# Optimization experiments

Hardware: AMD Instinct MI355X
Metric: run time of the kernel (lower is better)

Reference implementation:

```python
import jax, jax.numpy as jnp
import numpy as np
from jax import lax

DIM = 512
HEADS = 8
DIM_HEAD = 64          # dim // 8
LANDMARKS = 256        # dim // 2
PINV_ITERS = 6
KERNEL = 33            # residual depthwise conv kernel (lucidrains default)
LN_EPS = 1e-5


def setup_inputs() -> dict:
    key = jax.random.key(0)
    ks = jax.random.split(key, 5)
    b, n = 4, 8192
    x = jax.random.normal(ks[0], (b, n, DIM), jnp.float32)
    ln_w = jnp.ones((DIM,), jnp.float32)
    ln_b = jnp.zeros((DIM,), jnp.float32)
    w_qkv = jax.random.normal(ks[1], (DIM, 3 * HEADS * DIM_HEAD), jnp.float32) * (DIM ** -0.5)
    w_out = jax.random.normal(ks[2], (HEADS * DIM_HEAD, DIM), jnp.float32) * (DIM ** -0.5)
    b_out = jnp.zeros((DIM,), jnp.float32)
    conv_w = jax.random.normal(ks[3], (HEADS, 1, KERNEL, 1), jnp.float32) * 0.05
    return {"x": x, "ln_w": ln_w, "ln_b": ln_b, "w_qkv": w_qkv,
            "w_out": w_out, "b_out": b_out, "conv_w": conv_w}


def _moore_penrose_pinv(a, iters):
    # iterative Moore-Penrose pseudoinverse (Ben-Israel/Cohen cubic scheme)
    abs_a = jnp.abs(a)
    # global max over all batch/head slices, matching torch.max(col)*torch.max(row)
    scale = jnp.max(abs_a.sum(-1)) * jnp.max(abs_a.sum(-2))
    z = jnp.swapaxes(a, -1, -2) / scale
    I = jnp.eye(a.shape[-1], dtype=a.dtype)
    for _ in range(iters):
        az = a @ z
        z = 0.25 * (z @ (13.0 * I - az @ (11.0 * I - az @ (7.0 * I - az))))
    return z


def reference(x, ln_w, ln_b, w_qkv, w_out, b_out, conv_w):
    b, n, d = x.shape
    h, dh, m = HEADS, DIM_HEAD, LANDMARKS
    # --- LayerNorm ---
    mu = jnp.mean(x, -1, keepdims=True)
    var = jnp.mean((x - mu) ** 2, -1, keepdims=True)
    xn = (x - mu) * lax.rsqrt(var + LN_EPS) * ln_w + ln_b
    # --- pad front so seq divisible by num_landmarks (static; 0 here) ---
    pad = (-n) % m
    xp = jnp.pad(xn, ((0, 0), (pad, 0), (0, 0)))
    npad = n + pad
    # --- qkv projections ---
    qkv = xp @ w_qkv                      # (b, npad, 3*h*dh)
    q, k, v = jnp.split(qkv, 3, axis=-1)
    to_heads = lambda t: t.reshape(b, npad, h, dh).transpose(0, 2, 1, 3)  # bhnd
    q = to_heads(q) * (dh ** -0.5)
    k = to_heads(k)
    v = to_heads(v)
    # --- landmarks: mean over contiguous blocks of length l ---
    l = npad // m
    q_l = q.reshape(b, h, m, l, dh).mean(3)   # (b,h,m,dh)
    k_l = k.reshape(b, h, m, l, dh).mean(3)
    # --- three similarity/softmax blocks ---
    a1 = jax.nn.softmax(jnp.einsum('bhid,bhjd->bhij', q, k_l), -1)   # (b,h,n,m)
    a2 = jax.nn.softmax(jnp.einsum('bhid,bhjd->bhij', q_l, k_l), -1) # (b,h,m,m)
    a3 = jax.nn.softmax(jnp.einsum('bhid,bhjd->bhij', q_l, k), -1)   # (b,h,m,n)
    out = (a1 @ _moore_penrose_pinv(a2, PINV_ITERS)) @ (a3 @ v)      # (b,h,n,dh)
    # --- depthwise conv residual on v along sequence axis ---
    res = lax.conv_general_dilated(
        v, conv_w, window_strides=(1, 1),
        padding=((KERNEL // 2, KERNEL // 2), (0, 0)),
        dimension_numbers=('NCHW', 'OIHW', 'NCHW'),
        feature_group_count=h)
    out = out + res
    # --- merge heads, output projection, strip pad (dropout = identity in eval) ---
    out = out.transpose(0, 2, 1, 3).reshape(b, npad, h * dh)
    out = out @ w_out + b_out
    out = out[:, npad - n:]
    # --- TransLayer residual ---
    return x + out
```

## Files before the change

### kernel.cpp

```cpp
#include <hip/hip_runtime.h>

#define DEV __device__ __forceinline__

typedef unsigned short u16;
typedef unsigned int   u32;
typedef u16   u16x8 __attribute__((ext_vector_type(8)));
typedef __bf16 bf16x8 __attribute__((ext_vector_type(8)));
typedef float f32x4 __attribute__((ext_vector_type(4)));

DEV float b2f(u16 u){ return __uint_as_float(((u32)u) << 16); }
DEV u16 f2b(float f){ u32 u = __float_as_uint(f); u32 r = (u + 0x7fffu + ((u >> 16) & 1u)) >> 16; return (u16)r; }

DEV f32x4 mfma16(u16x8 a, u16x8 b, f32x4 c){
  return __builtin_amdgcn_mfma_f32_16x16x32_bf16(
      __builtin_bit_cast(bf16x8, a), __builtin_bit_cast(bf16x8, b), c, 0, 0, 0);
}

DEV void gload16(const void* g, void* l){
  __builtin_amdgcn_global_load_lds(
      (const __attribute__((address_space(1))) u32*)g,
      (__attribute__((address_space(3))) u32*)l,
      16, 0, 0);
}

__global__ __launch_bounds__(256) void ln_kernel(const float* __restrict__ x,
                                                 const float* __restrict__ w,
                                                 const float* __restrict__ bb,
                                                 u16* __restrict__ xn,
                                                 float2* __restrict__ stats){
  int row = blockIdx.x;
  const float* xr = x + (size_t)row * 512;
  int t = threadIdx.x;
  float2 v = *(const float2*)(xr + t * 2);
  float s = v.x + v.y;
  float sq = v.x * v.x + v.y * v.y;
  #pragma unroll
  for(int off = 32; off; off >>= 1){ s += __shfl_xor(s, off, 64); sq += __shfl_xor(sq, off, 64); }
  __shared__ float rs[4], rq[4];
  int wv = t >> 6, ln = t & 63;
  if(ln == 0){ rs[wv] = s; rq[wv] = sq; }
  __syncthreads();
  s = rs[0] + rs[1] + rs[2] + rs[3];
  sq = rq[0] + rq[1] + rq[2] + rq[3];
  float mu = s * (1.f / 512.f);
  float var = sq * (1.f / 512.f) - mu * mu;
  float rstd = rsqrtf(var + 1e-5f);
  if(t == 0) stats[row] = make_float2(mu, rstd);
  float w0 = w[t * 2], w1 = w[t * 2 + 1], b0 = bb[t * 2], b1 = bb[t * 2 + 1];
  u16 u0 = f2b((v.x - mu) * rstd * w0 + b0);
  u16 u1 = f2b((v.y - mu) * rstd * w1 + b1);
  ((u32*)(xn + (size_t)row * 512))[t] = (u32)u0 | ((u32)u1 << 16);
}

__global__ __launch_bounds__(256) void xl_kernel(const float* __restrict__ x,
                                                 const float2* __restrict__ stats,
                                                 const float* __restrict__ w,
                                                 const float* __restrict__ bb,
                                                 float* __restrict__ xl){
  int blk = blockIdx.x;
  int b = blk >> 8, j = blk & 255;
  int t = threadIdx.x;
  int d0 = t * 2;
  float acc0 = 0.f, acc1 = 0.f;
  size_t row0 = (size_t)b * 8192 + (size_t)j * 32;
  for(int tt = 0; tt < 32; tt++){
    size_t row = row0 + tt;
    float2 st = stats[row];
    const float* xr = x + row * 512;
    float2 v = *(const float2*)(xr + d0);
    acc0 += (v.x - st.x) * st.y;
    acc1 += (v.y - st.x) * st.y;
  }
  float* dst = xl + (size_t)blk * 512;
  dst[d0]     = acc0 * (1.f / 32.f) * w[d0]     + bb[d0];
  dst[d0 + 1] = acc1 * (1.f / 32.f) * w[d0 + 1] + bb[d0 + 1];
}

__global__ __launch_bounds__(256) void prep_weights(const float* __restrict__ w_qkv,
                                                    const float* __restrict__ w_out,
                                                    u16* __restrict__ wqkvT,
                                                    u16* __restrict__ woutT,
                                                    float* __restrict__ wqkT){
  int idx = blockIdx.x * 256 + threadIdx.x;
  if(idx < 786432){
    int k = idx / 1536, n = idx - k * 1536;
    wqkvT[(size_t)n * 512 + k] = f2b(w_qkv[idx]);
  } else if(idx < 786432 + 262144){
    int i2 = idx - 786432;
    int k = i2 >> 9, n = i2 & 511;
    woutT[(size_t)n * 512 + k] = f2b(w_out[i2]);
  } else {
    int i3 = idx - 786432 - 262144;
    int n = i3 >> 9, k = i3 & 511;
    wqkT[i3] = w_qkv[(size_t)k * 1536 + n];
  }
}

__global__ __launch_bounds__(256) void vtrans_kernel(const u16* __restrict__ v,
                                                     u16* __restrict__ vt){
  __shared__ u16 tile[64][72];
  int bh = blockIdx.y, n0 = blockIdx.x * 64;
  int t = threadIdx.x;
  for(int s = t; s < 512; s += 256){
    int row = s >> 3, col = (s & 7) * 8;
    *(u16x8*)&tile[row][col] = *(const u16x8*)(v + ((size_t)bh * 8192 + n0 + row) * 64 + col);
  }
  __syncthreads();
  for(int s = t; s < 512; s += 256){
    int d = s >> 3, nc = (s & 7) * 8;
    u16x8 u;
    #pragma unroll
    for(int e = 0; e < 8; e++) u[e] = tile[nc + e][d];
    *(u16x8*)(vt + ((size_t)bh * 64 + d) * 8192 + n0 + nc) = u;
  }
}

template<int EPI>
__global__ __launch_bounds__(256) void gemm128(const u16* __restrict__ A,
                                               const u16* __restrict__ BT,
                                               u16* __restrict__ qo, u16* __restrict__ ko, u16* __restrict__ vo,
                                               const float* __restrict__ bout,
                                               const float* __restrict__ xres,
                                               float* __restrict__ dout){
  __shared__ u16 As[128 * 32];
  __shared__ u16 Bs[128 * 32];
  const int K = 512;
  int nby = gridDim.y;
  int nwg = gridDim.x * nby;
  int orig = blockIdx.y * gridDim.x + blockIdx.x;
  int cpx = nwg >> 3;
  int wg = (orig & 7) * cpx + (orig >> 3);
  int fx = wg / nby, fy = wg - fx * nby;
  int tb_m = fx * 128, tb_n = fy * 128;
  int tid = threadIdx.x, lane = tid & 63, w = tid >> 6;
  int wm = (w >> 1) * 64, wn = (w & 1) * 64;
  f32x4 acc[4][4] = {};
  int srow = tid >> 2, sk = (tid & 3) * 8;
  const u16* Ag = A + (size_t)(tb_m + srow) * K + sk;
  const u16* Bg = BT + (size_t)(tb_n + srow) * K + sk;
  u16* Al = As + tid * 8;
  u16* Bl = Bs + tid * 8;
  for(int kk = 0; kk < K; kk += 32){
    __syncthreads();
    gload16(Ag + kk, Al);
    gload16(Ag + kk + (size_t)64 * K, Al + 2048);
    gload16(Bg + kk, Bl);
    gload16(Bg + kk + (size_t)64 * K, Bl + 2048);
    __syncthreads();
    int r = lane & 15, ko2 = (lane >> 4) * 8;
    u16x8 af[4], bf[4];
    #pragma unroll
    for(int mi = 0; mi < 4; mi++) af[mi] = *(const u16x8*)&As[(wm + mi * 16 + r) * 32 + ko2];
    #pragma unroll
    for(int ni = 0; ni < 4; ni++) bf[ni] = *(const u16x8*)&Bs[(wn + ni * 16 + r) * 32 + ko2];
    #pragma unroll
    for(int mi = 0; mi < 4; mi++)
      #pragma unroll
      for(int ni = 0; ni < 4; ni++)
        acc[mi][ni] = mfma16(af[mi], bf[ni], acc[mi][ni]);
  }
  int r = lane & 15, rr = (lane >> 4) * 4;
  #pragma unroll
  for(int mi = 0; mi < 4; mi++)
    #pragma unroll
    for(int ni = 0; ni < 4; ni++){
      int col = tb_n + wn + ni * 16 + r;
      #pragma unroll
      for(int e = 0; e < 4; e++){
        int row = tb_m + wm + mi * 16 + rr + e;
        float val = acc[mi][ni][e];
        if(EPI == 0){
          int t3 = col >> 9, h = (col >> 6) & 7, dh = col & 63;
          int b = row >> 13, n = row & 8191;
          if(t3 == 0) val *= 0.125f;
          u16* dst = (t3 == 0 ? qo : (t3 == 1 ? ko : vo));
          dst[(((size_t)(b * 8 + h) * 8192) + n) * 64 + dh] = f2b(val);
        } else {
          val += bout[col] + xres[(size_t)row * 512 + col];
          dout[(size_t)row * 512 + col] = val;
        }
      }
    }
}

__global__ __launch_bounds__(256) void gemm_qlkl(const float* __restrict__ A,
                                                 const float* __restrict__ BT,
                                                 float* __restrict__ qlf,
                                                 float* __restrict__ klf,
                                                 u16* __restrict__ qlh, u16* __restrict__ qll,
                                                 u16* __restrict__ klh, u16* __restrict__ kll){
  __shared__ float As[64][17];
  __shared__ float Bs[64][17];
  int tb_m = blockIdx.x * 64, tb_n = blockIdx.y * 64;
  int tid = threadIdx.x;
  int ty = tid >> 4, tx = tid & 15;
  float acc[4][4] = {};
  int srow = tid >> 2, sseg = (tid & 3) * 4;
  const float* Ag = A + (size_t)(tb_m + srow) * 512 + sseg;
  const float* Bg = BT + (size_t)(tb_n + srow) * 512 + sseg;
  for(int kk = 0; kk < 512; kk += 16){
    __syncthreads();
    f32x4 a4 = *(const f32x4*)(Ag + kk);
    f32x4 b4 = *(const f32x4*)(Bg + kk);
    #pragma unroll
    for(int e = 0; e < 4; e++){ As[srow][sseg + e] = a4[e]; Bs[srow][sseg + e] = b4[e]; }
    __syncthreads();
    #pragma unroll
    for(int k2 = 0; k2 < 16; k2++){
      float a[4], b[4];
      #pragma unroll
      for(int i = 0; i < 4; i++) a[i] = As[ty * 4 + i][k2];
      #pragma unroll
      for(int jv = 0; jv < 4; jv++) b[jv] = Bs[tx * 4 + jv][k2];
      #pragma unroll
      for(int i = 0; i < 4; i++)
        #pragma unroll
        for(int jv = 0; jv < 4; jv++) acc[i][jv] += a[i] * b[jv];
    }
  }
  #pragma unroll
  for(int i = 0; i < 4; i++)
    #pragma unroll
    for(int jv = 0; jv < 4; jv++){
      int r = tb_m + ty * 4 + i;
      int c = tb_n + tx * 4 + jv;
      int b = r >> 8, jl = r & 255;
      float val = acc[i][jv];
      if(c < 512){
        float q = val * 0.125f;
        size_t qi = (((size_t)(b * 8 + (c >> 6)) * 256) + jl) * 64 + (c & 63);
        qlf[qi] = q;
        u16 hi = f2b(q);
        qlh[qi] = hi; qll[qi] = f2b(q - b2f(hi));
      } else {
        int c2 = c - 512;
        size_t ki = (((size_t)(b * 8 + (c2 >> 6)) * 256) + jl) * 64 + (c2 & 63);
        klf[ki] = val;
        u16 hi = f2b(val);
        klh[ki] = hi; kll[ki] = f2b(val - b2f(hi));
      }
    }
}

__global__ __launch_bounds__(256) void gemm_pinv_f32(const float* __restrict__ A,
                                                     const float* __restrict__ B,
                                                     float* __restrict__ C,
                                                     float dB, float sB, float osc){
  __shared__ float As[64][68];
  __shared__ float Bs[64][68];
  int bh = blockIdx.y;
  size_t base = (size_t)bh * 65536;
  int tb_m = (blockIdx.x >> 2) * 64, tb_n = (blockIdx.x & 3) * 64;
  int tid = threadIdx.x;
  int ty = tid >> 4, tx = tid & 15;
  float acc[4][4] = {};
  int arow = tid >> 2, acol = (tid & 3) * 16;
  int brow = tid >> 3, bcol = (tid & 7) * 8;
  const float* Ag = A + base + (size_t)(tb_m + arow) * 256 + acol;
  const float* Bg = B + base + (size_t)brow * 256 + tb_n + bcol;
  for(int kk = 0; kk < 256; kk += 64){
    f32x4 a[4];
    #pragma unroll
    for(int q = 0; q < 4; q++) a[q] = *(const f32x4*)(Ag + kk + q * 4);
    f32x4 b[2][2];
    #pragma unroll
    for(int rr = 0; rr < 2; rr++){
      const float* bp = Bg + (size_t)(kk + rr * 32) * 256;
      b[rr][0] = *(const f32x4*)bp;
      b[rr][1] = *(const f32x4*)(bp + 4);
    }
    __syncthreads();
    #pragma unroll
    for(int q = 0; q < 4; q++)
      #pragma unroll
      for(int e = 0; e < 4; e++)
        As[acol + q * 4 + e][arow] = a[q][e];
    #pragma unroll
    for(int rr = 0; rr < 2; rr++){
      int krow = kk + rr * 32 + brow;
      f32x4 v0, v1;
      #pragma unroll
      for(int e = 0; e < 4; e++){
        float t0 = sB * b[rr][0][e]; if(krow == tb_n + bcol + e)     t0 += dB;
        float t1 = sB * b[rr][1][e]; if(krow == tb_n + bcol + 4 + e) t1 += dB;
        v0[e] = t0; v1[e] = t1;
      }
      *(f32x4*)&Bs[rr * 32 + brow][bcol]     = v0;
      *(f32x4*)&Bs[rr * 32 + brow][bcol + 4] = v1;
    }
    __syncthreads();
    #pragma unroll
    for(int k2 = 0; k2 < 64; k2++){
      f32x4 av4 = *(const f32x4*)&As[k2][ty * 4];
      f32x4 bv4 = *(const f32x4*)&Bs[k2][tx * 4];
      #pragma unroll
      for(int i = 0; i < 4; i++)
        #pragma unroll
        for(int jv = 0; jv < 4; jv++) acc[i][jv] += av4[i] * bv4[jv];
    }
  }
  #pragma unroll
  for(int i = 0; i < 4; i++){
    int r = tb_m + ty * 4 + i;
    f32x4 ov;
    #pragma unroll
    for(int jv = 0; jv < 4; jv++) ov[jv] = osc * acc[i][jv];
    *(f32x4*)(C + base + (size_t)r * 256 + tb_n + tx * 4) = ov;
  }
}

__global__ __launch_bounds__(256) void a2_kernel(const float* __restrict__ qlf,
                                                 const float* __restrict__ klf,
                                                 float* __restrict__ a2){
  int i = blockIdx.x, bh = blockIdx.y, j = threadIdx.x;
  const float* qp = qlf + ((size_t)bh * 256 + i) * 64;
  const float* kp = klf + ((size_t)bh * 256 + j) * 64;
  float s = 0.f;
  #pragma unroll
  for(int d0 = 0; d0 < 16; d0++){
    f32x4 uq = *(const f32x4*)(qp + d0 * 4);
    f32x4 uk = *(const f32x4*)(kp + d0 * 4);
    #pragma unroll
    for(int e = 0; e < 4; e++) s += uq[e] * uk[e];
  }
  __shared__ float red[256];
  red[j] = s; __syncthreads();
  for(int off = 128; off; off >>= 1){ if(j < off) red[j] = fmaxf(red[j], red[j + off]); __syncthreads(); }
  float m = red[0]; __syncthreads();
  float p = expf(s - m);
  red[j] = p; __syncthreads();
  for(int off = 128; off; off >>= 1){ if(j < off) red[j] += red[j + off]; __syncthreads(); }
  float denom = red[0];
  a2[((size_t)bh * 256 + i) * 256 + j] = p / denom;
}

__global__ __launch_bounds__(256) void scale_kernel(const float* __restrict__ a2, u32* __restrict__ maxes){
  int bh = blockIdx.x, t = threadIdx.x;
  const float* p = a2 + (size_t)bh * 65536;
  float cs = 0.f, rs = 0.f;
  for(int i = 0; i < 256; i++) cs += p[i * 256 + t];
  for(int j = 0; j < 256; j++) rs += p[t * 256 + j];
  __shared__ float rc[256], rr[256];
  rc[t] = cs; rr[t] = rs; __syncthreads();
  for(int off = 128; off; off >>= 1){
    if(t < off){ rc[t] = fmaxf(rc[t], rc[t + off]); rr[t] = fmaxf(rr[t], rr[t + off]); }
    __syncthreads();
  }
  if(t == 0){
    atomicMax(&maxes[0], __float_as_uint(rc[0]));
    atomicMax(&maxes[1], __float_as_uint(rr[0]));
  }
}

__global__ __launch_bounds__(256) void z0_kernel(const float* __restrict__ a2,
                                                 float* __restrict__ z,
                                                 const u32* __restrict__ maxes){
  __shared__ float tile[64][65];
  float inv = 1.f / (__uint_as_float(maxes[0]) * __uint_as_float(maxes[1]));
  int bh = blockIdx.z;
  int i0 = blockIdx.x * 64, j0 = blockIdx.y * 64;
  const float* src = a2 + (size_t)bh * 65536;
  float* dst = z + (size_t)bh * 65536;
  for(int s = threadIdx.x; s < 1024; s += 256){
    int r = s >> 4, c4 = (s & 15) * 4;
    f32x4 v = *(const f32x4*)(src + (size_t)(i0 + r) * 256 + j0 + c4);
    #pragma unroll
    for(int e = 0; e < 4; e++) tile[r][c4 + e] = v[e];
  }
  __syncthreads();
  for(int s = threadIdx.x; s < 1024; s += 256){
    int jr = s >> 4, c4 = (s & 15) * 4;
    f32x4 v;
    #pragma unroll
    for(int e = 0; e < 4; e++) v[e] = tile[c4 + e][jr] * inv;
    *(f32x4*)(dst + (size_t)(j0 + jr) * 256 + i0 + c4) = v;
  }
}

template<int MODE>
__global__ __launch_bounds__(256) void flash_kernel(
    const u16* __restrict__ Aex,
    const u16* __restrict__ Ah_, const u16* __restrict__ Al_,
    const u16* __restrict__ Bh_, const u16* __restrict__ Bl_,
    const u16* __restrict__ Vh_, const u16* __restrict__ Vl_,
    u16* __restrict__ o,
    float* __restrict__ pacc, float* __restrict__ plo){
  extern __shared__ char smem[];
  u32 (*pbuf)[32][35] = (u32(*)[32][35])smem;
  u16 (*ksh)[72] = (u16(*)[72])(smem + 17920);
  u16 (*vsh)[72] = (u16(*)[72])(smem + 17920 + 9216);
  u16 (*ksl)[72] = (u16(*)[72])(smem + 17920 + 2 * 9216);
  u16 (*vsl)[72] = (u16(*)[72])(smem + 17920 + 3 * 9216);

  int tid = threadIdx.x;
  int w = tid >> 6, lane = tid & 63;
  int lr = lane & 15, lg = lane >> 4;
  int bh = blockIdx.y;
  int rowbase = blockIdx.x * 128 + w * 32;
  constexpr int NT = (MODE == 0) ? 4 : 8;
  int kbase = (MODE == 0) ? 0 : blockIdx.z * 512;
  int srow = tid >> 2, sseg = (tid & 3) * 16;

  u16x8 afh[2][2], afl[2][2];
  #pragma unroll
  for(int mi = 0; mi < 2; mi++)
    #pragma unroll
    for(int ks = 0; ks < 2; ks++){
      int r = rowbase + mi * 16 + lr;
      if(MODE == 0){
        afh[mi][ks] = *(const u16x8*)(Aex + ((size_t)bh * 8192 + r) * 64 + ks * 32 + lg * 8);
      } else {
        size_t idx = ((size_t)bh * 256 + r) * 64 + ks * 32 + lg * 8;
        afh[mi][ks] = *(const u16x8*)(Ah_ + idx);
        afl[mi][ks] = *(const u16x8*)(Al_ + idx);
      }
    }

  f32x4 pv[2][4] = {};
  float l[2][4] = {};

  for(int t = 0; t < NT; t++){
    int koff = t * 64;
    __syncthreads();
    if(MODE == 0){
      size_t kix = ((size_t)bh * 256 + koff + srow) * 64 + sseg;
      *(u16x8*)&ksh[srow][sseg]     = *(const u16x8*)(Bh_ + kix);
      *(u16x8*)&ksh[srow][sseg + 8] = *(const u16x8*)(Bh_ + kix + 8);
      *(u16x8*)&ksl[srow][sseg]     = *(const u16x8*)(Bl_ + kix);
      *(u16x8*)&ksl[srow][sseg + 8] = *(const u16x8*)(Bl_ + kix + 8);
      size_t vix = ((size_t)bh * 64 + srow) * 256 + koff + sseg;
      *(u16x8*)&vsh[srow][sseg]     = *(const u16x8*)(Vh_ + vix);
      *(u16x8*)&vsh[srow][sseg + 8] = *(const u16x8*)(Vh_ + vix + 8);
      *(u16x8*)&vsl[srow][sseg]     = *(const u16x8*)(Vl_ + vix);
      *(u16x8*)&vsl[srow][sseg + 8] = *(const u16x8*)(Vl_ + vix + 8);
    } else {
      size_t kix = ((size_t)bh * 8192 + kbase + koff + srow) * 64 + sseg;
      *(u16x8*)&ksh[srow][sseg]     = *(const u16x8*)(Bh_ + kix);
      *(u16x8*)&ksh[srow][sseg + 8] = *(const u16x8*)(Bh_ + kix + 8);
      size_t vix = ((size_t)bh * 64 + srow) * 8192 + kbase + koff + sseg;
      *(u16x8*)&vsh[srow][sseg]     = *(const u16x8*)(Vh_ + vix);
      *(u16x8*)&vsh[srow][sseg + 8] = *(const u16x8*)(Vh_ + vix + 8);
    }
    __syncthreads();
    #pragma unroll
    for(int half = 0; half < 2; half++){
      u16x8 bfh[2][2], bfl[2][2];
      #pragma unroll
      for(int ni = 0; ni < 2; ni++){
        int krow = half * 32 + ni * 16 + lr;
        #pragma unroll
        for(int ks = 0; ks < 2; ks++){
          bfh[ni][ks] = *(const u16x8*)&ksh[krow][ks * 32 + lg * 8];
          if(MODE == 0) bfl[ni][ks] = *(const u16x8*)&ksl[krow][ks * 32 + lg * 8];
        }
      }
      f32x4 sv[2][2];
      #pragma unroll
      for(int mi = 0; mi < 2; mi++)
        #pragma unroll
        for(int ni = 0; ni < 2; ni++) sv[mi][ni] = (f32x4){0.f, 0.f, 0.f, 0.f};
      #pragma unroll
      for(int ks = 0; ks < 2; ks++)
        #pragma unroll
        for(int mi = 0; mi < 2; mi++)
          #pragma unroll
          for(int ni = 0; ni < 2; ni++){
            sv[mi][ni] = mfma16(afh[mi][ks], bfh[ni][ks], sv[mi][ni]);
            if(MODE == 0) sv[mi][ni] = mfma16(afh[mi][ks], bfl[ni][ks], sv[mi][ni]);
            else          sv[mi][ni] = mfma16(afl[mi][ks], bfh[ni][ks], sv[mi][ni]);
          }
      #pragma unroll
      for(int mi = 0; mi < 2; mi++)
        #pragma unroll
        for(int ni = 0; ni < 2; ni++)
          #pragma unroll
          for(int e = 0; e < 4; e++){
            float p = __expf(sv[mi][ni][e]);
            l[mi][e] += p;
            u32 pb = __float_as_uint(p);
            u32 rb = pb + 0x7fffu + ((pb >> 16) & 1u);
            float hif = __uint_as_float(rb & 0xffff0000u);
            u32 lob = __float_as_uint(p - hif);
            pbuf[w][mi * 16 + lg * 4 + e][ni * 16 + lr] = __builtin_amdgcn_perm(lob, rb, 0x07060302u);
          }
      u16x8 pah[2], pal[2];
      #pragma unroll
      for(int mi = 0; mi < 2; mi++){
        u32 tv[8];
        #pragma unroll
        for(int e2 = 0; e2 < 8; e2++) tv[e2] = pbuf[w][mi * 16 + lr][lg * 8 + e2];
        u32* ph = (u32*)&pah[mi];
        u32* pl = (u32*)&pal[mi];
        #pragma unroll
        for(int q = 0; q < 4; q++){
          ph[q] = __builtin_amdgcn_perm(tv[2 * q + 1], tv[2 * q], 0x05040100u);
          pl[q] = __builtin_amdgcn_perm(tv[2 * q + 1], tv[2 * q], 0x07060302u);
        }
      }
      #pragma unroll
      for(int ni2 = 0; ni2 < 4; ni2++){
        int d = ni2 * 16 + lr;
        u16x8 vh = *(const u16x8*)&vsh[d][half * 32 + lg * 8];
        u16x8 vl;
        if(MODE == 0) vl = *(const u16x8*)&vsl[d][half * 32 + lg * 8];
        #pragma unroll
        for(int mi = 0; mi < 2; mi++){
          pv[mi][ni2] = mfma16(pah[mi], vh, pv[mi][ni2]);
          if(MODE == 0){
            pv[mi][ni2] = mfma16(pah[mi], vl, pv[mi][ni2]);
            pv[mi][ni2] = mfma16(pal[mi], vh, pv[mi][ni2]);
          } else {
            pv[mi][ni2] = mfma16(pal[mi], vh, pv[mi][ni2]);
          }
        }
      }
    }
  }
  #pragma unroll
  for(int mi = 0; mi < 2; mi++)
    #pragma unroll
    for(int e = 0; e < 4; e++){
      float lv = l[mi][e];
      #pragma unroll
      for(int off = 1; off < 16; off <<= 1) lv += __shfl_xor(lv, off, 64);
      l[mi][e] = lv;
    }
  #pragma unroll
  for(int mi = 0; mi < 2; mi++){
    #pragma unroll
    for(int e = 0; e < 4; e++){
      int row = rowbase + mi * 16 + lg * 4 + e;
      if(MODE == 0){
        float invl = 1.f / l[mi][e];
        int b = bh >> 3, h = bh & 7;
        #pragma unroll
        for(int ni2 = 0; ni2 < 4; ni2++){
          int col = ni2 * 16 + lr;
          size_t oi = ((size_t)b * 8192 + row) * 512 + h * 64 + col;
          o[oi] = f2b(pv[mi][ni2][e] * invl + b2f(o[oi]));
        }
      } else {
        #pragma unroll
        for(int ni2 = 0; ni2 < 4; ni2++){
          int col = ni2 * 16 + lr;
          pacc[(((size_t)blockIdx.z * 8192) + (size_t)bh * 256 + row) * 64 + col] = pv[mi][ni2][e];
        }
      }
    }
  }
  if(MODE == 1 && lr == 0){
    #pragma unroll
    for(int mi = 0; mi < 2; mi++)
      #pragma unroll
      for(int e = 0; e < 4; e++){
        int row = rowbase + mi * 16 + lg * 4 + e;
        plo[(size_t)blockIdx.z * 8192 + (size_t)bh * 256 + row] = l[mi][e];
      }
  }
}

__global__ __launch_bounds__(64) void a3v_merge(const float* __restrict__ pacc,
                                                const float* __restrict__ plo,
                                                float* __restrict__ av){
  int row = blockIdx.x, d = threadIdx.x;
  float L = 0.f, acc = 0.f;
  #pragma unroll
  for(int p = 0; p < 16; p++){
    L += plo[(size_t)p * 8192 + row];
    acc += pacc[((size_t)p * 8192 + row) * 64 + d];
  }
  av[(size_t)row * 64 + d] = acc / L;
}

__global__ __launch_bounds__(64) void zw_kernel(const float* __restrict__ z,
                                                const float* __restrict__ av,
                                                u16* __restrict__ wth, u16* __restrict__ wtl){
  int i = blockIdx.x & 255, bh = blockIdx.x >> 8, d = threadIdx.x;
  const float* zr = z + ((size_t)bh * 256 + i) * 256;
  const float* ab = av + (size_t)bh * 256 * 64;
  float s = 0.f;
  for(int j = 0; j < 256; j++) s += zr[j] * ab[j * 64 + d];
  size_t oi = ((size_t)bh * 64 + d) * 256 + i;
  u16 hi = f2b(s);
  wth[oi] = hi;
  wtl[oi] = f2b(s - b2f(hi));
}

__global__ __launch_bounds__(256) void conv_kernel(const u16* __restrict__ v,
                                                   const float* __restrict__ cw,
                                                   u16* __restrict__ o){
  __shared__ float wl[33];
  __shared__ float vt[64][104];
  int bh = blockIdx.y, b = bh >> 3, h = bh & 7;
  int r0 = blockIdx.x * 64;
  if(threadIdx.x < 33) wl[threadIdx.x] = cw[h * 33 + threadIdx.x];
  const u16* vb = v + (size_t)bh * 8192 * 64;
  for(int idx = threadIdx.x; idx < 768; idx += 256){
    int row = idx >> 3, c8 = (idx & 7) * 8;
    int gr = r0 - 16 + row;
    u16x8 u = {};
    if(gr >= 0 && gr < 8192) u = *(const u16x8*)(vb + (size_t)gr * 64 + c8);
    #pragma unroll
    for(int e = 0; e < 8; e++) vt[c8 + e][row] = b2f(u[e]);
  }
  __syncthreads();
  int d = threadIdx.x & 63, g = threadIdx.x >> 6;
  float vin[48];
  #pragma unroll
  for(int i = 0; i < 12; i++){
    f32x4 q4 = *(const f32x4*)&vt[d][g * 16 + i * 4];
    #pragma unroll
    for(int e = 0; e < 4; e++) vin[i * 4 + e] = q4[e];
  }
  float acc[16] = {};
  #pragma unroll
  for(int t = 0; t < 33; t++){
    float wt = wl[t];
    #pragma unroll
    for(int r = 0; r < 16; r++) acc[r] += wt * vin[r + t];
  }
  #pragma unroll
  for(int r = 0; r < 16; r++){
    size_t oi = ((size_t)b * 8192 + (r0 + g * 16 + r)) * 512 + h * 64 + d;
    o[oi] = f2b(acc[r]);
  }
}

extern "C" void kernel_launch(void* const* d_in, const int* in_sizes, int n_in,
                              void* d_out, int out_size, void* d_ws, size_t ws_size,
                              hipStream_t stream){
  (void)in_sizes; (void)n_in; (void)out_size; (void)ws_size;
  const float* x     = (const float*)d_in[0];
  const float* ln_w  = (const float*)d_in[1];
  const float* ln_b  = (const float*)d_in[2];
  const float* w_qkv = (const float*)d_in[3];
  const float* w_out = (const float*)d_in[4];
  const float* b_out = (const float*)d_in[5];
  const float* cw    = (const float*)d_in[6];
  float* out = (float*)d_out;

  char* base = (char*)d_ws;
  size_t off = 0;
  auto alloc = [&](size_t bytes)->void*{
    void* r = base + off; off += (bytes + 255) & ~(size_t)255; return r;
  };
  u16* xn      = (u16*)alloc(32768ull * 512 * 2);
  float2* stat = (float2*)alloc(32768ull * 8);
  u16* qb      = (u16*)alloc(32ull * 8192 * 64 * 2);
  u16* kb      = (u16*)alloc(32ull * 8192 * 64 * 2);
  u16* vb      = (u16*)alloc(32ull * 8192 * 64 * 2);
  u16* vtb     = (u16*)alloc(32ull * 8192 * 64 * 2);
  u16* wqkvT   = (u16*)alloc(1536ull * 512 * 2);
  u16* woutT   = (u16*)alloc(512ull * 512 * 2);
  float* wqkT  = (float*)alloc(1024ull * 512 * 4);
  float* xl    = (float*)alloc(1024ull * 512 * 4);
  float* qlf   = (float*)alloc(32ull * 256 * 64 * 4);
  float* klf   = (float*)alloc(32ull * 256 * 64 * 4);
  u16* qlh     = (u16*)alloc(32ull * 256 * 64 * 2);
  u16* qll     = (u16*)alloc(32ull * 256 * 64 * 2);
  u16* klh     = (u16*)alloc(32ull * 256 * 64 * 2);
  u16* kll     = (u16*)alloc(32ull * 256 * 64 * 2);
  float* a2b   = (float*)alloc(32ull * 65536 * 4);
  float* zA    = (float*)alloc(32ull * 65536 * 4);
  float* zB    = (float*)alloc(32ull * 65536 * 4);
  float* az    = (float*)alloc(32ull * 65536 * 4);
  float* x2    = (float*)alloc(32ull * 65536 * 4);
  float* x3    = (float*)alloc(32ull * 65536 * 4);
  float* av    = (float*)alloc(32ull * 256 * 64 * 4);
  u16* wth     = (u16*)alloc(32ull * 64 * 256 * 2);
  u16* wtl     = (u16*)alloc(32ull * 64 * 256 * 2);
  u32* scal    = (u32*)alloc(256);
  u16* ob = xn;
  float* pacc = zB;
  float* plo  = a2b;

  hipMemsetAsync(scal, 0, 8, stream);
  ln_kernel<<<32768, 256, 0, stream>>>(x, ln_w, ln_b, xn, stat);
  prep_weights<<<6144, 256, 0, stream>>>(w_qkv, w_out, wqkvT, woutT, wqkT);
  gemm128<0><<<dim3(256, 12), 256, 0, stream>>>(xn, wqkvT, qb, kb, vb, nullptr, nullptr, nullptr);
  vtrans_kernel<<<dim3(128, 32), 256, 0, stream>>>(vb, vtb);
  xl_kernel<<<1024, 256, 0, stream>>>(x, stat, ln_w, ln_b, xl);
  gemm_qlkl<<<dim3(16, 16), 256, 0, stream>>>(xl, wqkT, qlf, klf, qlh, qll, klh, kll);
  a2_kernel<<<dim3(256, 32), 256, 0, stream>>>(qlf, klf, a2b);
  scale_kernel<<<32, 256, 0, stream>>>(a2b, scal);
  z0_kernel<<<dim3(4, 4, 32), 256, 0, stream>>>(a2b, zA, scal);

  float* zP = zA; float* zQ = zB;
  for(int it = 0; it < 6; it++){
    gemm_pinv_f32<<<dim3(16, 32), 256, 0, stream>>>(a2b, zP, az, 0.f, 1.f, 1.f);
    gemm_pinv_f32<<<dim3(16, 32), 256, 0, stream>>>(az, az, x2, 7.f, -1.f, 1.f);
    gemm_pinv_f32<<<dim3(16, 32), 256, 0, stream>>>(az, x2, x3, 11.f, -1.f, 1.f);
    gemm_pinv_f32<<<dim3(16, 32), 256, 0, stream>>>(zP, x3, zQ, 13.f, -1.f, 0.25f);
    float* t1 = zP; zP = zQ; zQ = t1;
  }

  flash_kernel<1><<<dim3(2, 32, 16), 256, 36352, stream>>>(nullptr, qlh, qll, kb, nullptr, vtb, nullptr,
                                                           nullptr, pacc, plo);
  a3v_merge<<<8192, 64, 0, stream>>>(pacc, plo, av);
  zw_kernel<<<8192, 64, 0, stream>>>(zP, av, wth, wtl);
  conv_kernel<<<dim3(128, 32), 256, 0, stream>>>(vb, cw, ob);
  flash_kernel<0><<<dim3(64, 32), 256, 54784, stream>>>(qb, nullptr, nullptr, klh, kll, wth, wtl,
                                                        ob, nullptr, nullptr);
  gemm128<1><<<dim3(256, 4), 256, 0, stream>>>(ob, woutT, nullptr, nullptr, nullptr, b_out, x, out);
}
```

Measured before the change: 951.1 us.

## Run pinv GEMMs on bf16 MFMA with three-way split precision

```diff
diff --git a/kernel.cpp b/kernel.cpp
--- a/kernel.cpp
+++ b/kernel.cpp
@@ -4,12 +4,26 @@
 
 typedef unsigned short u16;
 typedef unsigned int   u32;
+typedef u16   u16x4 __attribute__((ext_vector_type(4)));
 typedef u16   u16x8 __attribute__((ext_vector_type(8)));
 typedef __bf16 bf16x8 __attribute__((ext_vector_type(8)));
 typedef float f32x4 __attribute__((ext_vector_type(4)));
 
 DEV float b2f(u16 u){ return __uint_as_float(((u32)u) << 16); }
 DEV u16 f2b(float f){ u32 u = __float_as_uint(f); u32 r = (u + 0x7fffu + ((u >> 16) & 1u)) >> 16; return (u16)r; }
+
+DEV void split3(float x, u16& h, u16& l, u16& l2){
+  u32 ub = __float_as_uint(x);
+  u32 rb = ub + 0x7fffu + ((ub >> 16) & 1u);
+  float hf = __uint_as_float(rb & 0xffff0000u);
+  float r1 = x - hf;
+  u32 u1 = __float_as_uint(r1);
+  u32 rb1 = u1 + 0x7fffu + ((u1 >> 16) & 1u);
+  float lf = __uint_as_float(rb1 & 0xffff0000u);
+  h = (u16)(rb >> 16);
+  l = (u16)(rb1 >> 16);
+  l2 = f2b(r1 - lf);
+}
 
 DEV f32x4 mfma16(u16x8 a, u16x8 b, f32x4 c){
   return __builtin_amdgcn_mfma_f32_16x16x32_bf16(
@@ -242,76 +256,87 @@
     }
 }
 
-__global__ __launch_bounds__(256) void gemm_pinv_f32(const float* __restrict__ A,
-                                                     const float* __restrict__ B,
-                                                     float* __restrict__ C,
-                                                     float dB, float sB, float osc){
-  __shared__ float As[64][68];
-  __shared__ float Bs[64][68];
+__global__ __launch_bounds__(256) void gemm_pinv_mfma(
+    const u16* __restrict__ Ah, const u16* __restrict__ Al, const u16* __restrict__ Al2,
+    const u16* __restrict__ Bh, const u16* __restrict__ Bl, const u16* __restrict__ Bl2,
+    u16* __restrict__ Ch, u16* __restrict__ Cl, u16* __restrict__ Cl2,
+    float dB, int bneg, float osc){
+  __shared__ u16 As_[3][64][40];
+  __shared__ u16 Bs_[3][64][40];
   int bh = blockIdx.y;
   size_t base = (size_t)bh * 65536;
   int tb_m = (blockIdx.x >> 2) * 64, tb_n = (blockIdx.x & 3) * 64;
-  int tid = threadIdx.x;
-  int ty = tid >> 4, tx = tid & 15;
-  float acc[4][4] = {};
-  int arow = tid >> 2, acol = (tid & 3) * 16;
-  int brow = tid >> 3, bcol = (tid & 7) * 8;
-  const float* Ag = A + base + (size_t)(tb_m + arow) * 256 + acol;
-  const float* Bg = B + base + (size_t)brow * 256 + tb_n + bcol;
-  for(int kk = 0; kk < 256; kk += 64){
-    f32x4 a[4];
-    #pragma unroll
-    for(int q = 0; q < 4; q++) a[q] = *(const f32x4*)(Ag + kk + q * 4);
-    f32x4 b[2][2];
-    #pragma unroll
-    for(int rr = 0; rr < 2; rr++){
-      const float* bp = Bg + (size_t)(kk + rr * 32) * 256;
-      b[rr][0] = *(const f32x4*)bp;
-      b[rr][1] = *(const f32x4*)(bp + 4);
-    }
-    __syncthreads();
-    #pragma unroll
-    for(int q = 0; q < 4; q++)
-      #pragma unroll
-      for(int e = 0; e < 4; e++)
-        As[acol + q * 4 + e][arow] = a[q][e];
-    #pragma unroll
-    for(int rr = 0; rr < 2; rr++){
-      int krow = kk + rr * 32 + brow;
-      f32x4 v0, v1;
+  int tid = threadIdx.x, lane = tid & 63, w = tid >> 6;
+  int lr = lane & 15, lg = lane >> 4;
+  int wm = (w >> 1) * 32, wn = (w & 1) * 32;
+  f32x4 acc[2][2] = {};
+  int arow = tid >> 2, akq = (tid & 3) * 8;
+  int bcol = tid & 63, bkq = tid >> 6;
+  u16 sx = bneg ? (u16)0x8000u : (u16)0;
+  size_t aoff = base + (size_t)(tb_m + arow) * 256 + akq;
+  size_t boff = base + (size_t)(tb_n + bcol);
+  for(int kk = 0; kk < 256; kk += 32){
+    u16x8 ra0 = *(const u16x8*)(Ah + aoff + kk);
+    u16x8 ra1 = *(const u16x8*)(Al + aoff + kk);
+    u16x8 ra2 = *(const u16x8*)(Al2 + aoff + kk);
+    u16x8 rb0, rb1, rb2;
+    #pragma unroll
+    for(int j = 0; j < 8; j++){
+      size_t bi = boff + (size_t)(kk + bkq * 8 + j) * 256;
+      rb0[j] = Bh[bi] ^ sx;
+      rb1[j] = Bl[bi] ^ sx;
+      rb2[j] = Bl2[bi] ^ sx;
+    }
+    __syncthreads();
+    *(u16x8*)&As_[0][arow][akq] = ra0;
+    *(u16x8*)&As_[1][arow][akq] = ra1;
+    *(u16x8*)&As_[2][arow][akq] = ra2;
+    *(u16x8*)&Bs_[0][bcol][bkq * 8] = rb0;
+    *(u16x8*)&Bs_[1][bcol][bkq * 8] = rb1;
+    *(u16x8*)&Bs_[2][bcol][bkq * 8] = rb2;
+    __syncthreads();
+    u16x8 af[3][2], bf[3][2];
+    #pragma unroll
+    for(int v = 0; v < 3; v++)
+      #pragma unroll
+      for(int mi = 0; mi < 2; mi++){
+        af[v][mi] = *(const u16x8*)&As_[v][wm + mi * 16 + lr][lg * 8];
+        bf[v][mi] = *(const u16x8*)&Bs_[v][wn + mi * 16 + lr][lg * 8];
+      }
+    #pragma unroll
+    for(int mi = 0; mi < 2; mi++)
+      #pragma unroll
+      for(int ni = 0; ni < 2; ni++){
+        acc[mi][ni] = mfma16(af[1][mi], bf[1][ni], acc[mi][ni]);
+        acc[mi][ni] = mfma16(af[2][mi], bf[0][ni], acc[mi][ni]);
+        acc[mi][ni] = mfma16(af[0][mi], bf[2][ni], acc[mi][ni]);
+        acc[mi][ni] = mfma16(af[1][mi], bf[0][ni], acc[mi][ni]);
+        acc[mi][ni] = mfma16(af[0][mi], bf[1][ni], acc[mi][ni]);
+        acc[mi][ni] = mfma16(af[0][mi], bf[0][ni], acc[mi][ni]);
+      }
+  }
+  #pragma unroll
+  for(int mi = 0; mi < 2; mi++)
+    #pragma unroll
+    for(int ni = 0; ni < 2; ni++)
       #pragma unroll
       for(int e = 0; e < 4; e++){
-        float t0 = sB * b[rr][0][e]; if(krow == tb_n + bcol + e)     t0 += dB;
-        float t1 = sB * b[rr][1][e]; if(krow == tb_n + bcol + 4 + e) t1 += dB;
-        v0[e] = t0; v1[e] = t1;
-      }
-      *(f32x4*)&Bs[rr * 32 + brow][bcol]     = v0;
-      *(f32x4*)&Bs[rr * 32 + brow][bcol + 4] = v1;
-    }
-    __syncthreads();
-    #pragma unroll
-    for(int k2 = 0; k2 < 64; k2++){
-      f32x4 av4 = *(const f32x4*)&As[k2][ty * 4];
-      f32x4 bv4 = *(const f32x4*)&Bs[k2][tx * 4];
-      #pragma unroll
-      for(int i = 0; i < 4; i++)
-        #pragma unroll
-        for(int jv = 0; jv < 4; jv++) acc[i][jv] += av4[i] * bv4[jv];
-    }
-  }
-  #pragma unroll
-  for(int i = 0; i < 4; i++){
-    int r = tb_m + ty * 4 + i;
-    f32x4 ov;
-    #pragma unroll
-    for(int jv = 0; jv < 4; jv++) ov[jv] = osc * acc[i][jv];
-    *(f32x4*)(C + base + (size_t)r * 256 + tb_n + tx * 4) = ov;
-  }
+        int r = tb_m + wm + mi * 16 + lg * 4 + e;
+        int c = tb_n + wn + ni * 16 + lr;
+        size_t idx = base + (size_t)r * 256 + c;
+        float arec = b2f(Ah[idx]) + b2f(Al[idx]) + b2f(Al2[idx]);
+        float val = osc * (dB * arec + acc[mi][ni][e]);
+        u16 h, l, l2;
+        split3(val, h, l, l2);
+        Ch[idx] = h; Cl[idx] = l; Cl2[idx] = l2;
+      }
 }
 
 __global__ __launch_bounds__(256) void a2_kernel(const float* __restrict__ qlf,
                                                  const float* __restrict__ klf,
-                                                 float* __restrict__ a2){
+                                                 float* __restrict__ a2,
+                                                 u16* __restrict__ a2h, u16* __restrict__ a2l,
+                                                 u16* __restrict__ a2l2){
   int i = blockIdx.x, bh = blockIdx.y, j = threadIdx.x;
   const float* qp = qlf + ((size_t)bh * 256 + i) * 64;
   const float* kp = klf + ((size_t)bh * 256 + j) * 64;
@@ -331,7 +356,12 @@
   red[j] = p; __syncthreads();
   for(int off = 128; off; off >>= 1){ if(j < off) red[j] += red[j + off]; __syncthreads(); }
   float denom = red[0];
-  a2[((size_t)bh * 256 + i) * 256 + j] = p / denom;
+  float vv = p / denom;
+  size_t idx = ((size_t)bh * 256 + i) * 256 + j;
+  a2[idx] = vv;
+  u16 h, l, l2;
+  split3(vv, h, l, l2);
+  a2h[idx] = h; a2l[idx] = l; a2l2[idx] = l2;
 }
 
 __global__ __launch_bounds__(256) void scale_kernel(const float* __restrict__ a2, u32* __restrict__ maxes){
@@ -353,14 +383,15 @@
 }
 
 __global__ __launch_bounds__(256) void z0_kernel(const float* __restrict__ a2,
-                                                 float* __restrict__ z,
+                                                 u16* __restrict__ zh, u16* __restrict__ zl,
+                                                 u16* __restrict__ zl2,
                                                  const u32* __restrict__ maxes){
   __shared__ float tile[64][65];
   float inv = 1.f / (__uint_as_float(maxes[0]) * __uint_as_float(maxes[1]));
   int bh = blockIdx.z;
   int i0 = blockIdx.x * 64, j0 = blockIdx.y * 64;
   const float* src = a2 + (size_t)bh * 65536;
-  float* dst = z + (size_t)bh * 65536;
+  size_t dbase = (size_t)bh * 65536;
   for(int s = threadIdx.x; s < 1024; s += 256){
     int r = s >> 4, c4 = (s & 15) * 4;
     f32x4 v = *(const f32x4*)(src + (size_t)(i0 + r) * 256 + j0 + c4);
@@ -370,10 +401,18 @@
   __syncthreads();
   for(int s = threadIdx.x; s < 1024; s += 256){
     int jr = s >> 4, c4 = (s & 15) * 4;
-    f32x4 v;
-    #pragma unroll
-    for(int e = 0; e < 4; e++) v[e] = tile[c4 + e][jr] * inv;
-    *(f32x4*)(dst + (size_t)(j0 + jr) * 256 + i0 + c4) = v;
+    u16x4 hv, lv, l2v;
+    #pragma unroll
+    for(int e = 0; e < 4; e++){
+      float val = tile[c4 + e][jr] * inv;
+      u16 h, l, l2;
+      split3(val, h, l, l2);
+      hv[e] = h; lv[e] = l; l2v[e] = l2;
+    }
+    size_t doff = dbase + (size_t)(j0 + jr) * 256 + i0 + c4;
+    *(u16x4*)(zh + doff) = hv;
+    *(u16x4*)(zl + doff) = lv;
+    *(u16x4*)(zl2 + doff) = l2v;
   }
 }
 
@@ -572,14 +611,25 @@
   av[(size_t)row * 64 + d] = acc / L;
 }
 
-__global__ __launch_bounds__(64) void zw_kernel(const float* __restrict__ z,
+__global__ __launch_bounds__(64) void zw_kernel(const u16* __restrict__ zh,
+                                                const u16* __restrict__ zl,
+                                                const u16* __restrict__ zl2,
                                                 const float* __restrict__ av,
                                                 u16* __restrict__ wth, u16* __restrict__ wtl){
   int i = blockIdx.x & 255, bh = blockIdx.x >> 8, d = threadIdx.x;
-  const float* zr = z + ((size_t)bh * 256 + i) * 256;
+  size_t zr = ((size_t)bh * 256 + i) * 256;
   const float* ab = av + (size_t)bh * 256 * 64;
   float s = 0.f;
-  for(int j = 0; j < 256; j++) s += zr[j] * ab[j * 64 + d];
+  for(int j8 = 0; j8 < 32; j8++){
+    u16x8 hv = *(const u16x8*)(zh + zr + j8 * 8);
+    u16x8 lv = *(const u16x8*)(zl + zr + j8 * 8);
+    u16x8 l2v = *(const u16x8*)(zl2 + zr + j8 * 8);
+    #pragma unroll
+    for(int e = 0; e < 8; e++){
+      float zv = b2f(hv[e]) + b2f(lv[e]) + b2f(l2v[e]);
+      s += zv * ab[(j8 * 8 + e) * 64 + d];
+    }
+  }
   size_t oi = ((size_t)bh * 64 + d) * 256 + i;
   u16 hi = f2b(s);
   wth[oi] = hi;
@@ -644,6 +694,7 @@
   auto alloc = [&](size_t bytes)->void*{
     void* r = base + off; off += (bytes + 255) & ~(size_t)255; return r;
   };
+  const size_t MSZ = 32ull * 65536 * 2;
   u16* xn      = (u16*)alloc(32768ull * 512 * 2);
   float2* stat = (float2*)alloc(32768ull * 8);
   u16* qb      = (u16*)alloc(32ull * 8192 * 64 * 2);
@@ -656,23 +707,36 @@
   float* xl    = (float*)alloc(1024ull * 512 * 4);
   float* qlf   = (float*)alloc(32ull * 256 * 64 * 4);
   float* klf   = (float*)alloc(32ull * 256 * 64 * 4);
+  float* a2b   = (float*)alloc(32ull * 65536 * 4);
   u16* qlh     = (u16*)alloc(32ull * 256 * 64 * 2);
   u16* qll     = (u16*)alloc(32ull * 256 * 64 * 2);
   u16* klh     = (u16*)alloc(32ull * 256 * 64 * 2);
   u16* kll     = (u16*)alloc(32ull * 256 * 64 * 2);
-  float* a2b   = (float*)alloc(32ull * 65536 * 4);
-  float* zA    = (float*)alloc(32ull * 65536 * 4);
-  float* zB    = (float*)alloc(32ull * 65536 * 4);
-  float* az    = (float*)alloc(32ull * 65536 * 4);
-  float* x2    = (float*)alloc(32ull * 65536 * 4);
-  float* x3    = (float*)alloc(32ull * 65536 * 4);
+  u16* a2th    = (u16*)alloc(MSZ);
+  u16* a2tl    = (u16*)alloc(MSZ);
+  u16* a2tl2   = (u16*)alloc(MSZ);
+  u16* zAh     = (u16*)alloc(MSZ);
+  u16* zAl     = (u16*)alloc(MSZ);
+  u16* zAl2    = (u16*)alloc(MSZ);
+  u16* zBh     = (u16*)alloc(MSZ);
+  u16* zBl     = (u16*)alloc(MSZ);
+  u16* zBl2    = (u16*)alloc(MSZ);
   float* av    = (float*)alloc(32ull * 256 * 64 * 4);
   u16* wth     = (u16*)alloc(32ull * 64 * 256 * 2);
   u16* wtl     = (u16*)alloc(32ull * 64 * 256 * 2);
   u32* scal    = (u32*)alloc(256);
   u16* ob = xn;
-  float* pacc = zB;
-  float* plo  = a2b;
+  u16* azh  = xn;
+  u16* azl  = (u16*)((char*)xn + MSZ);
+  u16* azl2 = (u16*)((char*)xn + 2 * MSZ);
+  u16* x2h  = (u16*)((char*)xn + 3 * MSZ);
+  u16* x2l  = (u16*)((char*)xn + 4 * MSZ);
+  u16* x2l2 = (u16*)((char*)xn + 5 * MSZ);
+  u16* x3h  = (u16*)wqkT;
+  u16* x3l  = (u16*)((char*)wqkT + MSZ);
+  u16* x3l2 = (u16*)((char*)wqkT + 2 * MSZ);
+  float* pacc = (float*)xn;
+  float* plo  = (float*)wqkT;
 
   hipMemsetAsync(scal, 0, 8, stream);
   ln_kernel<<<32768, 256, 0, stream>>>(x, ln_w, ln_b, xn, stat);
@@ -681,23 +745,31 @@
   vtrans_kernel<<<dim3(128, 32), 256, 0, stream>>>(vb, vtb);
   xl_kernel<<<1024, 256, 0, stream>>>(x, stat, ln_w, ln_b, xl);
   gemm_qlkl<<<dim3(16, 16), 256, 0, stream>>>(xl, wqkT, qlf, klf, qlh, qll, klh, kll);
-  a2_kernel<<<dim3(256, 32), 256, 0, stream>>>(qlf, klf, a2b);
+  a2_kernel<<<dim3(256, 32), 256, 0, stream>>>(qlf, klf, a2b, a2th, a2tl, a2tl2);
   scale_kernel<<<32, 256, 0, stream>>>(a2b, scal);
-  z0_kernel<<<dim3(4, 4, 32), 256, 0, stream>>>(a2b, zA, scal);
-
-  float* zP = zA; float* zQ = zB;
+  z0_kernel<<<dim3(4, 4, 32), 256, 0, stream>>>(a2b, zAh, zAl, zAl2, scal);
+
+  u16* zPh = zAh; u16* zPl = zAl; u16* zPl2 = zAl2;
+  u16* zQh = zBh; u16* zQl = zBl; u16* zQl2 = zBl2;
   for(int it = 0; it < 6; it++){
-    gemm_pinv_f32<<<dim3(16, 32), 256, 0, stream>>>(a2b, zP, az, 0.f, 1.f, 1.f);
-    gemm_pinv_f32<<<dim3(16, 32), 256, 0, stream>>>(az, az, x2, 7.f, -1.f, 1.f);
-    gemm_pinv_f32<<<dim3(16, 32), 256, 0, stream>>>(az, x2, x3, 11.f, -1.f, 1.f);
-    gemm_pinv_f32<<<dim3(16, 32), 256, 0, stream>>>(zP, x3, zQ, 13.f, -1.f, 0.25f);
-    float* t1 = zP; zP = zQ; zQ = t1;
+    gemm_pinv_mfma<<<dim3(16, 32), 256, 0, stream>>>(a2th, a2tl, a2tl2, zPh, zPl, zPl2,
+                                                     azh, azl, azl2, 0.f, 0, 1.f);
+    gemm_pinv_mfma<<<dim3(16, 32), 256, 0, stream>>>(azh, azl, azl2, azh, azl, azl2,
+                                                     x2h, x2l, x2l2, 7.f, 1, 1.f);
+    gemm_pinv_mfma<<<dim3(16, 32), 256, 0, stream>>>(azh, azl, azl2, x2h, x2l, x2l2,
+                                                     x3h, x3l, x3l2, 11.f, 1, 1.f);
+    gemm_pinv_mfma<<<dim3(16, 32), 256, 0, stream>>>(zPh, zPl, zPl2, x3h, x3l, x3l2,
+                                                     zQh, zQl, zQl2, 13.f, 1, 0.25f);
+    u16* t;
+    t = zPh; zPh = zQh; zQh = t;
+    t = zPl; zPl = zQl; zQl = t;
+    t = zPl2; zPl2 = zQl2; zQl2 = t;
   }
 
   flash_kernel<1><<<dim3(2, 32, 16), 256, 36352, stream>>>(nullptr, qlh, qll, kb, nullptr, vtb, nullptr,
                                                            nullptr, pacc, plo);
   a3v_merge<<<8192, 64, 0, stream>>>(pacc, plo, av);
-  zw_kernel<<<8192, 64, 0, stream>>>(zP, av, wth, wtl);
+  zw_kernel<<<8192, 64, 0, stream>>>(zPh, zPl, zPl2, av, wth, wtl);
   conv_kernel<<<dim3(128, 32), 256, 0, stream>>>(vb, cw, ob);
   flash_kernel<0><<<dim3(64, 32), 256, 54784, stream>>>(qb, nullptr, nullptr, klh, kll, wth, wtl,
                                                         ob, nullptr, nullptr);
```

Result: faster. 930.9 us (-2.1%).
